# Kernel tuning notes

Hardware: AMD Instinct MI355X
Metric: run time of the kernel (lower is better)

## Reference

```python
import jax, jax.numpy as jnp
import numpy as np

BETA = 10.0
EXTREMA = 10.0
LIK_BOUND = 1e-9
FILTERS = (1, 3, 3, 3, 3, 1)


def _sos_tanh(xf, sos_w, sos_b):
    # xf: (C,1,L). Sum-of-tanh staircase quantizer (StanH):
    # y = -extrema + sum_i 0.5*w_i*(tanh(beta*(x-b_i))+1)
    t = jnp.tanh(BETA * (xf[..., None] - sos_b))  # (C,1,L,NS)
    return -EXTREMA + jnp.sum(0.5 * sos_w * (t + 1.0), axis=-1)


def _logits_cumulative(v, mats, biases, factors):
    # v: (C,1,L); per-channel MLP with softplus-reparameterized matrices
    logits = v
    for i, m in enumerate(mats):
        logits = jnp.einsum('coi,cil->col', jax.nn.softplus(m), logits) + biases[i]
        if i < len(factors):
            logits = logits + jnp.tanh(factors[i]) * jnp.tanh(logits)
    return logits


def setup_inputs() -> dict:
    key = jax.random.key(0)
    ks = jax.random.split(key, 8)
    N, C, H, W = 8, 192, 32, 32
    NS = 60
    x = jax.random.normal(ks[0], (N, C, H, W), jnp.float32) * 3.0
    # positive step weights summing roughly to the full range
    sos_w = jax.random.uniform(ks[1], (NS,), jnp.float32, 0.1, 1.0)
    sos_w = sos_w / jnp.sum(sos_w) * (2.0 * EXTREMA)
    sos_b = jnp.linspace(-EXTREMA, EXTREMA, NS).astype(jnp.float32)
    scale = 10.0 ** (1.0 / 5.0)
    out = {'x': x, 'sos_w': sos_w, 'sos_b': sos_b}
    kk = jax.random.split(ks[2], 10)
    for i in range(5):
        init = float(np.log(np.expm1(1.0 / scale / FILTERS[i + 1])))
        out[f'm{i}'] = jnp.full((C, FILTERS[i + 1], FILTERS[i]), init, jnp.float32)
        out[f'c{i}'] = jax.random.uniform(kk[i], (C, FILTERS[i + 1], 1), jnp.float32, -0.5, 0.5)
        if i < 4:
            out[f'f{i}'] = jnp.zeros((C, FILTERS[i + 1], 1), jnp.float32)
    return out


def reference(x, sos_w, sos_b, m0, m1, m2, m3, m4, c0, c1, c2, c3, c4, f0, f1, f2, f3):
    N, C, H, W = x.shape
    mats = (m0, m1, m2, m3, m4)
    biases = (c0, c1, c2, c3, c4)
    factors = (f0, f1, f2, f3)
    # permute (N,C,H,W) -> (C,1,N*H*W) as in quantize()
    xf = jnp.transpose(x, (1, 0, 2, 3)).reshape(C, 1, -1)
    yq = _sos_tanh(xf, sos_w, sos_b)  # training-mode SoS quantization
    lower = _logits_cumulative(yq - 0.5, mats, biases, factors)
    upper = _logits_cumulative(yq + 0.5, mats, biases, factors)
    sign = jax.lax.stop_gradient(-jnp.sign(lower + upper))
    lik = jnp.abs(jax.nn.sigmoid(sign * upper) - jax.nn.sigmoid(sign * lower))
    lik = jnp.maximum(lik, LIK_BOUND)
    y_hat = jnp.transpose(yq.reshape(C, N, H, W), (1, 0, 2, 3))
    lik = jnp.transpose(lik.reshape(C, N, H, W), (1, 0, 2, 3))
    return y_hat, lik
```

## Files before the change

kernel.cpp:

```cpp
#include <hip/hip_runtime.h>
#include <math.h>

#define C_CH    192
#define HW_     1024
#define NPLANE  1536
#define TOTAL_  1572864
#define PPB     2
#define NBLK    (NPLANE / PPB)

#define LOG2E   1.4426950408889634f
#define KSOS    28.853900817779268f
#define INV_D   2.95f

#define LUT_L   512
#define LUT_X0  (-10.72f)
#define LUT_SPAN 21.44f
#define LUT_H   (LUT_SPAN / (LUT_L - 1))
#define LUT_IH  ((LUT_L - 1) / LUT_SPAN)

__device__ __forceinline__ float rcp_f(float v)  { return __builtin_amdgcn_rcpf(v); }
__device__ __forceinline__ float exp2_f(float v) { return __builtin_amdgcn_exp2f(v); }

__device__ __forceinline__ float fast_tanh(float z) {
  float e = exp2_f(z * (2.0f * LOG2E));
  return 1.0f - 2.0f * rcp_f(e + 1.0f);
}
__device__ __forceinline__ float fast_sigmoid(float z) {
  return rcp_f(1.0f + exp2_f(-z * LOG2E));
}
__device__ __forceinline__ float softplus_f(float v) {
  return log1pf(expf(v));
}

__device__ __forceinline__ float mlp_full(float v, const float* P) {
  float t, a0, a1, a2, d0, d1, d2;
  t = fmaf(P[27], v, P[33]); a0 = fmaf(P[46], fast_tanh(t), t);
  t = fmaf(P[28], v, P[34]); a1 = fmaf(P[47], fast_tanh(t), t);
  t = fmaf(P[29], v, P[35]); a2 = fmaf(P[48], fast_tanh(t), t);

  t = fmaf(P[2], a2, fmaf(P[1], a1, fmaf(P[0], a0, P[36]))); d0 = fmaf(P[49], fast_tanh(t), t);
  t = fmaf(P[5], a2, fmaf(P[4], a1, fmaf(P[3], a0, P[37]))); d1 = fmaf(P[50], fast_tanh(t), t);
  t = fmaf(P[8], a2, fmaf(P[7], a1, fmaf(P[6], a0, P[38]))); d2 = fmaf(P[51], fast_tanh(t), t);

  t = fmaf(P[11], d2, fmaf(P[10], d1, fmaf(P[9],  d0, P[39]))); a0 = fmaf(P[52], fast_tanh(t), t);
  t = fmaf(P[14], d2, fmaf(P[13], d1, fmaf(P[12], d0, P[40]))); a1 = fmaf(P[53], fast_tanh(t), t);
  t = fmaf(P[17], d2, fmaf(P[16], d1, fmaf(P[15], d0, P[41]))); a2 = fmaf(P[54], fast_tanh(t), t);

  t = fmaf(P[20], a2, fmaf(P[19], a1, fmaf(P[18], a0, P[42]))); d0 = fmaf(P[55], fast_tanh(t), t);
  t = fmaf(P[23], a2, fmaf(P[22], a1, fmaf(P[21], a0, P[43]))); d1 = fmaf(P[56], fast_tanh(t), t);
  t = fmaf(P[26], a2, fmaf(P[25], a1, fmaf(P[24], a0, P[44]))); d2 = fmaf(P[57], fast_tanh(t), t);

  return fmaf(P[32], d2, fmaf(P[31], d1, fmaf(P[30], d0, P[45])));
}

__device__ __forceinline__ float mlp_fast(float v, const float* P) {
  float a0, a1, a2, d0, d1, d2;
  a0 = fmaf(P[27], v, P[33]);
  a1 = fmaf(P[28], v, P[34]);
  a2 = fmaf(P[29], v, P[35]);

  d0 = fmaf(P[2], a2, fmaf(P[1], a1, fmaf(P[0], a0, P[36])));
  d1 = fmaf(P[5], a2, fmaf(P[4], a1, fmaf(P[3], a0, P[37])));
  d2 = fmaf(P[8], a2, fmaf(P[7], a1, fmaf(P[6], a0, P[38])));

  a0 = fmaf(P[11], d2, fmaf(P[10], d1, fmaf(P[9],  d0, P[39])));
  a1 = fmaf(P[14], d2, fmaf(P[13], d1, fmaf(P[12], d0, P[40])));
  a2 = fmaf(P[17], d2, fmaf(P[16], d1, fmaf(P[15], d0, P[41])));

  d0 = fmaf(P[20], a2, fmaf(P[19], a1, fmaf(P[18], a0, P[42])));
  d1 = fmaf(P[23], a2, fmaf(P[22], a1, fmaf(P[21], a0, P[43])));
  d2 = fmaf(P[26], a2, fmaf(P[25], a1, fmaf(P[24], a0, P[44])));

  return fmaf(P[32], d2, fmaf(P[31], d1, fmaf(P[30], d0, P[45])));
}

template <bool FAST>
__device__ __forceinline__ float lik_from_y(float yq, const float* P) {
  float lo = FAST ? mlp_fast(yq - 0.5f, P) : mlp_full(yq - 0.5f, P);
  float up = FAST ? mlp_fast(yq + 0.5f, P) : mlp_full(yq + 0.5f, P);
  float lu = lo + up;
  float sg = (lu > 0.0f) ? -1.0f : ((lu < 0.0f) ? 1.0f : 0.0f);
  float lik = fabsf(fast_sigmoid(sg * up) - fast_sigmoid(sg * lo));
  return fmaxf(lik, 1e-9f);
}

__device__ __forceinline__ float sos5(
    float xx, const float* s_w, const float* s_kb, const float* s_pw)
{
  float kf = ceilf((xx + 9.15254237f) * INV_D);
  int k = (int)kf;
  k = max(0, min(60, k));
  float acc = s_pw[k];
  float kx  = KSOS * xx;
  #pragma unroll
  for (int i = 0; i < 5; ++i) {
    float z = s_kb[k + i] - kx;
    acc = fmaf(s_w[k + i], rcp_f(1.0f + exp2_f(z)), acc);
  }
  return acc - 10.0f;
}

__global__ __launch_bounds__(256)
void eb_fused3(const float* __restrict__ x,
               const float* __restrict__ sos_w, const float* __restrict__ sos_b,
               const float* __restrict__ m0, const float* __restrict__ m1,
               const float* __restrict__ m2, const float* __restrict__ m3,
               const float* __restrict__ m4,
               const float* __restrict__ c0, const float* __restrict__ c1,
               const float* __restrict__ c2, const float* __restrict__ c3,
               const float* __restrict__ c4,
               const float* __restrict__ f0, const float* __restrict__ f1,
               const float* __restrict__ f2, const float* __restrict__ f3,
               float* __restrict__ out)
{
  __shared__ float  s_w[68], s_kb[68], s_pw[64], s_p[58];
  __shared__ float2 s_yl[LUT_L];

  const int t  = threadIdx.x;
  const int c  = blockIdx.x % C_CH;
  const int g  = blockIdx.x / C_CH;
  const int base0 = ((2 * g)     * C_CH + c) * HW_;
  const int base1 = ((2 * g + 1) * C_CH + c) * HW_;

  float4 xv0 = reinterpret_cast<const float4*>(x + base0)[t];
  float4 xv1 = reinterpret_cast<const float4*>(x + base1)[t];

  const int p = t - 128;
  if (p >= 0 && p < 58) {
    float raw;
    if      (p <  9) raw = m1[c*9 +  p      ];
    else if (p < 18) raw = m2[c*9 + (p -  9)];
    else if (p < 27) raw = m3[c*9 + (p - 18)];
    else if (p < 30) raw = m0[c*3 + (p - 27)];
    else if (p < 33) raw = m4[c*3 + (p - 30)];
    else if (p < 36) raw = c0[c*3 + (p - 33)];
    else if (p < 39) raw = c1[c*3 + (p - 36)];
    else if (p < 42) raw = c2[c*3 + (p - 39)];
    else if (p < 45) raw = c3[c*3 + (p - 42)];
    else if (p < 46) raw = c4[c];
    else if (p < 49) raw = f0[c*3 + (p - 46)];
    else if (p < 52) raw = f1[c*3 + (p - 49)];
    else if (p < 55) raw = f2[c*3 + (p - 52)];
    else             raw = f3[c*3 + (p - 55)];
    float val;
    if      (p < 33) val = softplus_f(raw);
    else if (p < 46) val = raw;
    else             val = tanhf(raw);
    s_p[p] = val;
  }

  if (t < 68) {
    float w = (t < 60) ? sos_w[t] : 0.0f;
    float b = (t < 60) ? sos_b[t] : 0.0f;
    s_w[t]  = w;
    s_kb[t] = KSOS * b;
  }
  if (t >= 64 && t < 128) {
    int i = t - 64;
    float v = (i < 60) ? sos_w[i] : 0.0f;
    float s = v;
    #pragma unroll
    for (int off = 1; off < 64; off <<= 1) {
      float o = __shfl_up(s, off, 64);
      if (i >= off) s += o;
    }
    if (i <= 60) s_pw[i] = s - v;
  }
  __syncthreads();

  float P[58];
  #pragma unroll
  for (int i = 0; i < 58; ++i) P[i] = s_p[i];

  bool nofac = true;
  #pragma unroll
  for (int i = 46; i < 58; ++i) nofac &= (P[i] == 0.0f);

  if (nofac) {
    #pragma unroll
    for (int r = 0; r < LUT_L / 256; ++r) {
      int idx = t + 256 * r;
      float xg = LUT_X0 + (float)idx * LUT_H;
      float yq = sos5(xg, s_w, s_kb, s_pw);
      s_yl[idx] = make_float2(yq, lik_from_y<true>(yq, P));
    }
  } else {
    #pragma unroll
    for (int r = 0; r < LUT_L / 256; ++r) {
      int idx = t + 256 * r;
      float xg = LUT_X0 + (float)idx * LUT_H;
      float yq = sos5(xg, s_w, s_kb, s_pw);
      s_yl[idx] = make_float2(yq, lik_from_y<false>(yq, P));
    }
  }
  __syncthreads();

  float xsv[8] = {xv0.x, xv0.y, xv0.z, xv0.w, xv1.x, xv1.y, xv1.z, xv1.w};
  float ys[8], ls[8];
  #pragma unroll
  for (int e = 0; e < 8; ++e) {
    float xx = fminf(fmaxf(xsv[e], LUT_X0), LUT_X0 + LUT_SPAN);
    float u  = (xx - LUT_X0) * LUT_IH;
    int   i  = (int)u;
    i = min(i, LUT_L - 2);
    float fr = u - (float)i;
    float2 a = s_yl[i];
    float2 b = s_yl[i + 1];
    ys[e] = fmaf(fr, b.x - a.x, a.x);
    ls[e] = fmaf(fr, b.y - a.y, a.y);
  }

  reinterpret_cast<float4*>(out + base0)[t]          = make_float4(ys[0], ys[1], ys[2], ys[3]);
  reinterpret_cast<float4*>(out + base1)[t]          = make_float4(ys[4], ys[5], ys[6], ys[7]);
  reinterpret_cast<float4*>(out + TOTAL_ + base0)[t] = make_float4(ls[0], ls[1], ls[2], ls[3]);
  reinterpret_cast<float4*>(out + TOTAL_ + base1)[t] = make_float4(ls[4], ls[5], ls[6], ls[7]);
}

extern "C" void kernel_launch(void* const* d_in, const int* in_sizes, int n_in,
                              void* d_out, int out_size, void* d_ws, size_t ws_size,
                              hipStream_t stream) {
  const float* x  = (const float*)d_in[0];
  const float* sw = (const float*)d_in[1];
  const float* sb = (const float*)d_in[2];
  const float *M[5], *B[5], *F[4];

  if (n_in >= 17 && in_sizes[4] == 1728) {
    for (int i = 0; i < 5; ++i) M[i] = (const float*)d_in[3 + i];
    for (int i = 0; i < 5; ++i) B[i] = (const float*)d_in[8 + i];
    for (int i = 0; i < 4; ++i) F[i] = (const float*)d_in[13 + i];
  } else {
    M[0] = (const float*)d_in[3];  B[0] = (const float*)d_in[4];  F[0] = (const float*)d_in[5];
    M[1] = (const float*)d_in[6];  B[1] = (const float*)d_in[7];  F[1] = (const float*)d_in[8];
    M[2] = (const float*)d_in[9];  B[2] = (const float*)d_in[10]; F[2] = (const float*)d_in[11];
    M[3] = (const float*)d_in[12]; B[3] = (const float*)d_in[13]; F[3] = (const float*)d_in[14];
    M[4] = (const float*)d_in[15]; B[4] = (const float*)d_in[16];
  }

  hipLaunchKernelGGL(eb_fused3, dim3(NBLK), dim3(256), 0, stream,
                     x, sw, sb,
                     M[0], M[1], M[2], M[3], M[4],
                     B[0], B[1], B[2], B[3], B[4],
                     F[0], F[1], F[2], F[3],
                     (float*)d_out);
}
```

Baseline: 11.74 us.

## Use one plane per block and halve LUT size to one entry per thread

```diff
diff --git a/kernel.cpp b/kernel.cpp
--- a/kernel.cpp
+++ b/kernel.cpp
@@ -5,14 +5,13 @@
 #define HW_     1024
 #define NPLANE  1536
 #define TOTAL_  1572864
-#define PPB     2
-#define NBLK    (NPLANE / PPB)
+#define NBLK    NPLANE
 
 #define LOG2E   1.4426950408889634f
 #define KSOS    28.853900817779268f
 #define INV_D   2.95f
 
-#define LUT_L   512
+#define LUT_L   256
 #define LUT_X0  (-10.72f)
 #define LUT_SPAN 21.44f
 #define LUT_H   (LUT_SPAN / (LUT_L - 1))
@@ -101,7 +100,7 @@
 }
 
 __global__ __launch_bounds__(256)
-void eb_fused3(const float* __restrict__ x,
+void eb_fused4(const float* __restrict__ x,
                const float* __restrict__ sos_w, const float* __restrict__ sos_b,
                const float* __restrict__ m0, const float* __restrict__ m1,
                const float* __restrict__ m2, const float* __restrict__ m3,
@@ -116,14 +115,11 @@
   __shared__ float  s_w[68], s_kb[68], s_pw[64], s_p[58];
   __shared__ float2 s_yl[LUT_L];
 
-  const int t  = threadIdx.x;
-  const int c  = blockIdx.x % C_CH;
-  const int g  = blockIdx.x / C_CH;
-  const int base0 = ((2 * g)     * C_CH + c) * HW_;
-  const int base1 = ((2 * g + 1) * C_CH + c) * HW_;
-
-  float4 xv0 = reinterpret_cast<const float4*>(x + base0)[t];
-  float4 xv1 = reinterpret_cast<const float4*>(x + base1)[t];
+  const int t    = threadIdx.x;
+  const int c    = blockIdx.x % C_CH;
+  const int base = blockIdx.x * HW_;
+
+  float4 xv = reinterpret_cast<const float4*>(x + base)[t];
 
   const int p = t - 128;
   if (p >= 0 && p < 58) {
@@ -176,29 +172,18 @@
   #pragma unroll
   for (int i = 46; i < 58; ++i) nofac &= (P[i] == 0.0f);
 
-  if (nofac) {
-    #pragma unroll
-    for (int r = 0; r < LUT_L / 256; ++r) {
-      int idx = t + 256 * r;
-      float xg = LUT_X0 + (float)idx * LUT_H;
-      float yq = sos5(xg, s_w, s_kb, s_pw);
-      s_yl[idx] = make_float2(yq, lik_from_y<true>(yq, P));
-    }
-  } else {
-    #pragma unroll
-    for (int r = 0; r < LUT_L / 256; ++r) {
-      int idx = t + 256 * r;
-      float xg = LUT_X0 + (float)idx * LUT_H;
-      float yq = sos5(xg, s_w, s_kb, s_pw);
-      s_yl[idx] = make_float2(yq, lik_from_y<false>(yq, P));
-    }
+  {
+    float xg = LUT_X0 + (float)t * LUT_H;
+    float yq = sos5(xg, s_w, s_kb, s_pw);
+    float lk = nofac ? lik_from_y<true>(yq, P) : lik_from_y<false>(yq, P);
+    s_yl[t] = make_float2(yq, lk);
   }
   __syncthreads();
 
-  float xsv[8] = {xv0.x, xv0.y, xv0.z, xv0.w, xv1.x, xv1.y, xv1.z, xv1.w};
-  float ys[8], ls[8];
-  #pragma unroll
-  for (int e = 0; e < 8; ++e) {
+  float xsv[4] = {xv.x, xv.y, xv.z, xv.w};
+  float ys[4], ls[4];
+  #pragma unroll
+  for (int e = 0; e < 4; ++e) {
     float xx = fminf(fmaxf(xsv[e], LUT_X0), LUT_X0 + LUT_SPAN);
     float u  = (xx - LUT_X0) * LUT_IH;
     int   i  = (int)u;
@@ -210,10 +195,8 @@
     ls[e] = fmaf(fr, b.y - a.y, a.y);
   }
 
-  reinterpret_cast<float4*>(out + base0)[t]          = make_float4(ys[0], ys[1], ys[2], ys[3]);
-  reinterpret_cast<float4*>(out + base1)[t]          = make_float4(ys[4], ys[5], ys[6], ys[7]);
-  reinterpret_cast<float4*>(out + TOTAL_ + base0)[t] = make_float4(ls[0], ls[1], ls[2], ls[3]);
-  reinterpret_cast<float4*>(out + TOTAL_ + base1)[t] = make_float4(ls[4], ls[5], ls[6], ls[7]);
+  reinterpret_cast<float4*>(out + base)[t]          = make_float4(ys[0], ys[1], ys[2], ys[3]);
+  reinterpret_cast<float4*>(out + TOTAL_ + base)[t] = make_float4(ls[0], ls[1], ls[2], ls[3]);
 }
 
 extern "C" void kernel_launch(void* const* d_in, const int* in_sizes, int n_in,
@@ -236,7 +219,7 @@
     M[4] = (const float*)d_in[15]; B[4] = (const float*)d_in[16];
   }
 
-  hipLaunchKernelGGL(eb_fused3, dim3(NBLK), dim3(256), 0, stream,
+  hipLaunchKernelGGL(eb_fused4, dim3(NBLK), dim3(256), 0, stream,
                      x, sw, sb,
                      M[0], M[1], M[2], M[3], M[4],
                      B[0], B[1], B[2], B[3], B[4],
```

Result: slower. 12.63 us (+7.5%).
